# Performance work log

Measured on AMD Instinct MI355X. Metric: run time of the kernel, lower is better.

The kernel has to match this reference:

```python
import jax, jax.numpy as jnp
from jax import lax
import numpy as np

EPS = 1e-8


def setup_inputs() -> dict:
    key = jax.random.key(0)
    ks = jax.random.split(key, 9)
    B, T, E = 64, 256, 512
    L, H = 8, 512
    s = 0.05  # small init so gates are not saturated
    return {
        "x": jax.random.normal(ks[0], (B, T, E), jnp.float32),
        "w_ih": jax.random.normal(ks[1], (L, 4 * H, H), jnp.float32) * s,
        "w_hh": jax.random.normal(ks[2], (L, 4 * H, H), jnp.float32) * s,
        "b_ih": jax.random.normal(ks[3], (L, 4 * H), jnp.float32) * s,
        "b_hh": jax.random.normal(ks[4], (L, 4 * H), jnp.float32) * s,
        "ff1_w": jax.random.normal(ks[5], (H // 4, H), jnp.float32) * s,
        "ff1_b": jax.random.normal(ks[6], (H // 4,), jnp.float32) * s,
        "ff2_w": jax.random.normal(ks[7], (H // 16 * 2, H // 4), jnp.float32) * s,
        "ff2_b": jax.random.normal(ks[8], (H // 16 * 2,), jnp.float32) * s,
    }


def _lstm_layer(seq, W_ih, W_hh, bi, bh):
    # seq: [B, T, I]; PyTorch gate order: i, f, g, o
    B = seq.shape[0]
    H = W_hh.shape[1]
    pre = jnp.einsum('bti,gi->btg', seq, W_ih) + bi + bh  # [B, T, 4H]

    def step(carry, x_t):
        h, c = carry
        g = x_t + h @ W_hh.T  # [B, 4H]
        i, f, gg, o = jnp.split(g, 4, axis=-1)
        c = jax.nn.sigmoid(f) * c + jax.nn.sigmoid(i) * jnp.tanh(gg)
        h = jax.nn.sigmoid(o) * jnp.tanh(c)
        return (h, c), h

    h0 = jnp.zeros((B, H), seq.dtype)
    (hT, _), hs = lax.scan(step, (h0, h0), pre.transpose(1, 0, 2))
    return hs.transpose(1, 0, 2), hT  # [B,T,H], [B,H]


def reference(x, w_ih, w_hh, b_ih, b_hh, ff1_w, ff1_b, ff2_w, ff2_b):
    L = w_ih.shape[0]
    B = x.shape[0]
    seq = x
    finals = []
    for l in range(L):  # small fixed layer loop (sequential dependency)
        seq, hT = _lstm_layer(seq, w_ih[l], w_hh[l], b_ih[l], b_hh[l])
        finals.append(hT)
    h = jnp.stack(finals, axis=1)                # [B, L, H] == h.transpose(0,1)
    h = jax.nn.silu(h @ ff1_w.T + ff1_b)          # [B, L, H//4]
    h = h @ ff2_w.T + ff2_b                       # [B, L, H//16*2]
    h = h.reshape(B, -1)                          # [B, L*(H//16*2)]
    mean = h[:, ::2]
    log_var = h[:, 1::2]
    scale = jax.nn.softplus(log_var) + EPS        # diag of scale_tril
    return mean, scale
```

## Files before the change

kernel.cpp:

```cpp
#include <hip/hip_runtime.h>
#include <hip/hip_bf16.h>

typedef __bf16 bf16_t;
typedef __bf16 bf16x8 __attribute__((ext_vector_type(8)));
typedef float floatx4 __attribute__((ext_vector_type(4)));

#define LAYERS 8
#define BATCH  64
#define TSEQ   256
#define HDIM   512
#define GDIM   2048
#define UNITS  16
#define NROWS  64
#define WROW   1048
#define GROW   65
#define MAXM   257

#define W_OFF       0
#define W_BYTES     (NROWS * WROW * 2)
#define GATES_OFF   (W_OFF + W_BYTES)
#define GATES_BYTES (BATCH * GROW * 4)
#define C_OFF       (GATES_OFF + GATES_BYTES)
#define C_BYTES     (BATCH * UNITS * 4)
#define BIAS_OFF    (C_OFF + C_BYTES)
#define BIAS_BYTES  (NROWS * 4)
#define LDS_TOTAL   (BIAS_OFF + BIAS_BYTES)

__device__ __forceinline__ floatx4 mfma16(bf16x8 a, bf16x8 b, floatx4 c) {
    return __builtin_amdgcn_mfma_f32_16x16x32_bf16(a, b, c, 0, 0, 0);
}
__device__ __forceinline__ float sigm(float x) {
    return 1.0f / (1.0f + __expf(-x));
}
__device__ __forceinline__ unsigned pload(const unsigned* p) {
    return __hip_atomic_load(p, __ATOMIC_RELAXED, __HIP_MEMORY_SCOPE_AGENT);
}

__global__ void prep(const float* __restrict__ x, bf16_t* __restrict__ x_bf,
                     bf16_t* __restrict__ h_buf, unsigned* __restrict__ prog,
                     int M) {
    const int gtid = blockIdx.x * blockDim.x + threadIdx.x;
    const int nthr = gridDim.x * blockDim.x;
    for (int i = gtid; i < BATCH * TSEQ * HDIM; i += nthr) {
        int e = i & (HDIM - 1);
        int b = (i >> 9) & 63;
        int t = i >> 15;
        x_bf[i] = (bf16_t)x[((size_t)b * TSEQ + t) * HDIM + e];
    }
    const size_t lstride = (size_t)M * BATCH * HDIM;
    for (int i = gtid; i < LAYERS * BATCH * HDIM; i += nthr) {
        int l   = i / (BATCH * HDIM);
        int off = i % (BATCH * HDIM);
        h_buf[(size_t)l * lstride + off] = (bf16_t)0.0f;
    }
    for (int i = gtid; i < 256 * 16; i += nthr) prog[i] = 0u;
}

__global__ void lstm_main(const float* __restrict__ w_ih,
                          const float* __restrict__ w_hh,
                          const float* __restrict__ b_ih,
                          const float* __restrict__ b_hh,
                          const bf16_t* __restrict__ x_bf,
                          bf16_t* __restrict__ h_buf,
                          float*  __restrict__ finals,
                          unsigned* __restrict__ prog,
                          int M, int F)
{
    extern __shared__ char smem[];
    bf16_t* wlds  = (bf16_t*)(smem + W_OFF);
    float*  gates = (float*)(smem + GATES_OFF);
    float*  cst   = (float*)(smem + C_OFF);
    float*  bias  = (float*)(smem + BIAS_OFF);

    const int tid   = threadIdx.x;
    const int blk   = blockIdx.x;
    const int layer = blk & 7;
    const int slice = blk >> 3;
    const int u0    = slice * UNITS;
    const size_t lstride = (size_t)M * BATCH * HDIM;

    for (int r = 0; r < NROWS; ++r) {
        const int gate = ((r >> 4) * 512) + u0 + (r & 15);
        const float* srcA = w_ih + ((size_t)layer * GDIM + gate) * HDIM;
        const float* srcB = w_hh + ((size_t)layer * GDIM + gate) * HDIM;
        wlds[r * WROW + tid]       = (bf16_t)srcA[tid];
        wlds[r * WROW + 512 + tid] = (bf16_t)srcB[tid];
    }
    if (tid < NROWS) {
        const int gate = ((tid >> 4) * 512) + u0 + (tid & 15);
        bias[tid] = b_ih[layer * GDIM + gate] + b_hh[layer * GDIM + gate];
    }
    for (int i = tid; i < BATCH * UNITS; i += blockDim.x) cst[i] = 0.0f;
    __syncthreads();

    const int lane = tid & 63;
    const int wave = tid >> 6;
    const int quad = lane >> 4;
    const int l15  = lane & 15;
    const int m0   = (wave & 3) * 16;
    const int nb0  = (wave >> 2) * 32;
    const int arow = m0 + l15;
    const bf16_t* b_base0 = wlds + (size_t)(nb0 + l15) * WROW + quad * 8;
    const bf16_t* b_base1 = b_base0 + (size_t)16 * WROW;

    const int cb = tid >> 3;
    const int jp = tid & 7;
    const int i32 = tid & 31;

    for (int t = 0; t < TSEQ; ++t) {
        if (tid < 32) {
            if (layer > 0) {
                const unsigned* f = prog + ((i32 << 3) + layer - 1) * 16;
                while (pload(f) < (unsigned)(t + 1)) {}
            }
        } else if (tid >= 64 && tid < 96) {
            if (t > 0) {
                const unsigned* f = prog + ((i32 << 3) + layer) * 16;
                while (pload(f) < (unsigned)t) {}
            }
        } else if (tid >= 128 && tid < 160) {
            if (layer < 7 && t >= M - 1) {
                const unsigned* f = prog + ((i32 << 3) + layer + 1) * 16;
                while (pload(f) < (unsigned)(t - M + 2)) {}
            }
        }
        __builtin_amdgcn_fence(__ATOMIC_ACQUIRE, "workgroup");
        if ((t % F) == 0)
            __builtin_amdgcn_fence(__ATOMIC_ACQUIRE, "agent");
        __syncthreads();

        const int slot_w = (t + 1) % M;
        const int slot_o = t % M;
        const bf16_t* src_lo = (layer == 0)
            ? (x_bf + (size_t)t * BATCH * HDIM)
            : (h_buf + (size_t)(layer - 1) * lstride
                     + (size_t)slot_w * BATCH * HDIM);
        const bf16_t* src_hi =
            h_buf + (size_t)layer * lstride + (size_t)slot_o * BATCH * HDIM;

        const bf16_t* a_lo = src_lo + (size_t)arow * HDIM + quad * 8;
        const bf16_t* a_hi = src_hi + (size_t)arow * HDIM + quad * 8;

        floatx4 acc0 = {0.f, 0.f, 0.f, 0.f};
        floatx4 acc1 = {0.f, 0.f, 0.f, 0.f};

        #pragma unroll 4
        for (int kk = 0; kk < 16; ++kk) {
            bf16x8 a  = *(const bf16x8*)(a_lo + kk * 32);
            bf16x8 b0 = *(const bf16x8*)(b_base0 + kk * 32);
            bf16x8 b1 = *(const bf16x8*)(b_base1 + kk * 32);
            acc0 = mfma16(a, b0, acc0);
            acc1 = mfma16(a, b1, acc1);
        }
        #pragma unroll 4
        for (int kk = 0; kk < 16; ++kk) {
            bf16x8 a  = *(const bf16x8*)(a_hi + kk * 32);
            bf16x8 b0 = *(const bf16x8*)(b_base0 + 512 + kk * 32);
            bf16x8 b1 = *(const bf16x8*)(b_base1 + 512 + kk * 32);
            acc0 = mfma16(a, b0, acc0);
            acc1 = mfma16(a, b1, acc1);
        }

        #pragma unroll
        for (int r = 0; r < 4; ++r) {
            const int brow = m0 + quad * 4 + r;
            gates[brow * GROW + nb0 + l15]      = acc0[r];
            gates[brow * GROW + nb0 + 16 + l15] = acc1[r];
        }
        __syncthreads();

        {
            const int j0 = jp * 2, j1 = j0 + 1;
            const float* g = gates + cb * GROW;
            const float iv0 = g[j0]      + bias[j0];
            const float fv0 = g[16 + j0] + bias[16 + j0];
            const float gv0 = g[32 + j0] + bias[32 + j0];
            const float ov0 = g[48 + j0] + bias[48 + j0];
            const float iv1 = g[j1]      + bias[j1];
            const float fv1 = g[16 + j1] + bias[16 + j1];
            const float gv1 = g[32 + j1] + bias[32 + j1];
            const float ov1 = g[48 + j1] + bias[48 + j1];
            const float c0 = sigm(fv0) * cst[cb * UNITS + j0]
                           + sigm(iv0) * tanhf(gv0);
            const float c1 = sigm(fv1) * cst[cb * UNITS + j1]
                           + sigm(iv1) * tanhf(gv1);
            cst[cb * UNITS + j0] = c0;
            cst[cb * UNITS + j1] = c1;
            const float h0 = sigm(ov0) * tanhf(c0);
            const float h1 = sigm(ov1) * tanhf(c1);
            const bf16_t hb0 = (bf16_t)h0, hb1 = (bf16_t)h1;
            const uint32_t u =
                ((uint32_t)__builtin_bit_cast(unsigned short, hb1) << 16) |
                (uint32_t)__builtin_bit_cast(unsigned short, hb0);
            uint32_t* dst = (uint32_t*)(h_buf + (size_t)layer * lstride
                + ((size_t)slot_w * BATCH + cb) * HDIM + u0 + j0);
            __hip_atomic_store(dst, u, __ATOMIC_RELAXED,
                               __HIP_MEMORY_SCOPE_AGENT);
            if (t == TSEQ - 1) {
                float2 f2 = make_float2(h0, h1);
                *(float2*)(finals + ((size_t)cb * LAYERS + layer) * HDIM
                           + u0 + j0) = f2;
            }
        }
        __syncthreads();
        if (tid == 0)
            __hip_atomic_store(prog + blk * 16, (unsigned)(t + 1),
                               __ATOMIC_RELAXED, __HIP_MEMORY_SCOPE_AGENT);
    }
}

__global__ void ff_epilogue(const float* __restrict__ finals,
                            const float* __restrict__ ff1_w,
                            const float* __restrict__ ff1_b,
                            const float* __restrict__ ff2_w,
                            const float* __restrict__ ff2_b,
                            float* __restrict__ out)
{
    __shared__ float fin[HDIM];
    __shared__ float hid[128];
    const int blk = blockIdx.x;
    const int b = blk >> 3, l = blk & 7;
    const int tid = threadIdx.x;

    const float* frow = finals + ((size_t)b * LAYERS + l) * HDIM;
    for (int k = tid; k < HDIM; k += 128) fin[k] = frow[k];
    __syncthreads();

    float acc = ff1_b[tid];
    const float* w1 = ff1_w + (size_t)tid * HDIM;
    #pragma unroll 4
    for (int k = 0; k < HDIM; ++k) acc = fmaf(fin[k], w1[k], acc);
    hid[tid] = acc * (1.0f / (1.0f + __expf(-acc)));
    __syncthreads();

    if (tid < 64) {
        float o = ff2_b[tid];
        const float* w2 = ff2_w + (size_t)tid * 128;
        #pragma unroll 4
        for (int k = 0; k < 128; ++k) o = fmaf(hid[k], w2[k], o);
        const int j = l * 64 + tid;
        const int col = j >> 1;
        if ((j & 1) == 0) {
            out[b * 256 + col] = o;
        } else {
            const float sp = fmaxf(o, 0.0f) + log1pf(__expf(-fabsf(o)));
            out[64 * 256 + b * 256 + col] = sp + 1e-8f;
        }
    }
}

extern "C" void kernel_launch(void* const* d_in, const int* in_sizes, int n_in,
                              void* d_out, int out_size, void* d_ws, size_t ws_size,
                              hipStream_t stream) {
    const float* x     = (const float*)d_in[0];
    const float* w_ih  = (const float*)d_in[1];
    const float* w_hh  = (const float*)d_in[2];
    const float* b_ih  = (const float*)d_in[3];
    const float* b_hh  = (const float*)d_in[4];
    const float* ff1_w = (const float*)d_in[5];
    const float* ff1_b = (const float*)d_in[6];
    const float* ff2_w = (const float*)d_in[7];
    const float* ff2_b = (const float*)d_in[8];
    float* out = (float*)d_out;

    const size_t fixed = (size_t)TSEQ * BATCH * HDIM * 2
                       + (size_t)BATCH * LAYERS * HDIM * 4
                       + 256 * 16 * 4 + 4096;
    const size_t per_slot = (size_t)LAYERS * BATCH * HDIM * 2;
    int M = MAXM;
    if (ws_size > fixed) {
        size_t fit = (ws_size - fixed) / per_slot;
        if (fit < (size_t)M) M = (int)fit;
    }
    if (M < 5) M = 5;
    const int F = M - 1;

    char* ws = (char*)d_ws;
    bf16_t* x_bf = (bf16_t*)ws;
    size_t off = (size_t)TSEQ * BATCH * HDIM * 2;
    float* finals = (float*)(ws + off);
    off += (size_t)BATCH * LAYERS * HDIM * 4;
    unsigned* prog = (unsigned*)(ws + off);
    off += 256 * 16 * 4;
    off = (off + 255) & ~(size_t)255;
    bf16_t* h_buf = (bf16_t*)(ws + off);

    (void)in_sizes; (void)n_in; (void)out_size;

    hipFuncSetAttribute((const void*)lstm_main,
                        hipFuncAttributeMaxDynamicSharedMemorySize, LDS_TOTAL);

    prep<<<dim3(1024), dim3(256), 0, stream>>>(x, x_bf, h_buf, prog, M);

    void* args[] = {(void*)&w_ih, (void*)&w_hh, (void*)&b_ih, (void*)&b_hh,
                    (void*)&x_bf, (void*)&h_buf, (void*)&finals, (void*)&prog,
                    (void*)&M, (void*)&F};
    hipLaunchCooperativeKernel((const void*)lstm_main, dim3(256), dim3(512),
                               args, LDS_TOTAL, stream);

    ff_epilogue<<<dim3(512), dim3(128), 0, stream>>>(finals, ff1_w, ff1_b,
                                                     ff2_w, ff2_b, out);
}
```

Before: 3.036 ms.

## Split hidden-state exchange into intra-layer ring and cross-layer ring with separate flags

Separates the recurrent h exchange among blocks of the same layer (a small 16-slot ring with its own progress flags, polled using sc0 loads and stored at workgroup scope) from the cross-layer handoff (the large ring at agent scope, written only when another layer consumes it). The same-layer wait moves after the input-projection MFMA loop so the x·W_ih half overlaps with waiting on peers. The progress signal for the previous step is published early, at the start of the next step. It relies on same-layer blocks seeing each other's data through weaker scopes and cache bypass, which risks memory-ordering bugs, and it adds a second global store per element.

```diff
diff --git a/kernel.cpp b/kernel.cpp
--- a/kernel.cpp
+++ b/kernel.cpp
@@ -15,6 +15,7 @@
 #define WROW   1048
 #define GROW   65
 #define MAXM   257
+#define NSS    16
 
 #define W_OFF       0
 #define W_BYTES     (NROWS * WROW * 2)
@@ -32,13 +33,23 @@
 __device__ __forceinline__ float sigm(float x) {
     return 1.0f / (1.0f + __expf(-x));
 }
-__device__ __forceinline__ unsigned pload(const unsigned* p) {
+__device__ __forceinline__ unsigned pload_x(const unsigned* p) {
     return __hip_atomic_load(p, __ATOMIC_RELAXED, __HIP_MEMORY_SCOPE_AGENT);
 }
+__device__ __forceinline__ void pstore_x(unsigned* p, unsigned v) {
+    __hip_atomic_store(p, v, __ATOMIC_RELAXED, __HIP_MEMORY_SCOPE_AGENT);
+}
+__device__ __forceinline__ unsigned poll_s(const unsigned* p) {
+    unsigned v;
+    asm volatile("global_load_dword %0, %1, off sc0\n\t"
+                 "s_waitcnt vmcnt(0)"
+                 : "=v"(v) : "v"(p) : "memory");
+    return v;
+}
 
 __global__ void prep(const float* __restrict__ x, bf16_t* __restrict__ x_bf,
-                     bf16_t* __restrict__ h_buf, unsigned* __restrict__ prog,
-                     int M) {
+                     bf16_t* __restrict__ h_s, unsigned* __restrict__ prog_x,
+                     unsigned* __restrict__ prog_s) {
     const int gtid = blockIdx.x * blockDim.x + threadIdx.x;
     const int nthr = gridDim.x * blockDim.x;
     for (int i = gtid; i < BATCH * TSEQ * HDIM; i += nthr) {
@@ -47,13 +58,9 @@
         int t = i >> 15;
         x_bf[i] = (bf16_t)x[((size_t)b * TSEQ + t) * HDIM + e];
     }
-    const size_t lstride = (size_t)M * BATCH * HDIM;
-    for (int i = gtid; i < LAYERS * BATCH * HDIM; i += nthr) {
-        int l   = i / (BATCH * HDIM);
-        int off = i % (BATCH * HDIM);
-        h_buf[(size_t)l * lstride + off] = (bf16_t)0.0f;
-    }
-    for (int i = gtid; i < 256 * 16; i += nthr) prog[i] = 0u;
+    for (int i = gtid; i < LAYERS * NSS * BATCH * HDIM / 2; i += nthr)
+        ((unsigned*)h_s)[i] = 0u;
+    for (int i = gtid; i < 256 * 16; i += nthr) { prog_x[i] = 0u; prog_s[i] = 0u; }
 }
 
 __global__ void lstm_main(const float* __restrict__ w_ih,
@@ -61,9 +68,11 @@
                           const float* __restrict__ b_ih,
                           const float* __restrict__ b_hh,
                           const bf16_t* __restrict__ x_bf,
-                          bf16_t* __restrict__ h_buf,
+                          bf16_t* __restrict__ h_x,
+                          bf16_t* __restrict__ h_s,
                           float*  __restrict__ finals,
-                          unsigned* __restrict__ prog,
+                          unsigned* __restrict__ prog_x,
+                          unsigned* __restrict__ prog_s,
                           int M, int F)
 {
     extern __shared__ char smem[];
@@ -78,6 +87,7 @@
     const int slice = blk >> 3;
     const int u0    = slice * UNITS;
     const size_t lstride = (size_t)M * BATCH * HDIM;
+    const bool ringmode = (M < MAXM);
 
     for (int r = 0; r < NROWS; ++r) {
         const int gate = ((r >> 4) * 512) + u0 + (r & 15);
@@ -104,46 +114,33 @@
     const bf16_t* b_base1 = b_base0 + (size_t)16 * WROW;
 
     const int cb = tid >> 3;
-    const int jp = tid & 7;
+    const int jp = tid & 3 | ((tid & 7) & ~3);
     const int i32 = tid & 31;
 
     for (int t = 0; t < TSEQ; ++t) {
-        if (tid < 32) {
-            if (layer > 0) {
-                const unsigned* f = prog + ((i32 << 3) + layer - 1) * 16;
-                while (pload(f) < (unsigned)(t + 1)) {}
-            }
-        } else if (tid >= 64 && tid < 96) {
-            if (t > 0) {
-                const unsigned* f = prog + ((i32 << 3) + layer) * 16;
-                while (pload(f) < (unsigned)t) {}
-            }
-        } else if (tid >= 128 && tid < 160) {
-            if (layer < 7 && t >= M - 1) {
-                const unsigned* f = prog + ((i32 << 3) + layer + 1) * 16;
-                while (pload(f) < (unsigned)(t - M + 2)) {}
-            }
-        }
-        __builtin_amdgcn_fence(__ATOMIC_ACQUIRE, "workgroup");
-        if ((t % F) == 0)
+        if (layer > 0 && tid < 32) {
+            const unsigned* f = prog_x + ((i32 << 3) + layer - 1) * 16;
+            while ((int)(pload_x(f) - (unsigned)(t + 1)) < 0) {}
+        } else if (ringmode && layer < 7 && tid >= 128 && tid < 160 &&
+                   t >= M - 1) {
+            const unsigned* f = prog_x + ((i32 << 3) + layer + 1) * 16;
+            while ((int)(pload_x(f) - (unsigned)(t + 2 - M)) < 0) {}
+        }
+        __syncthreads();
+        if (ringmode && (t % F) == 0)
             __builtin_amdgcn_fence(__ATOMIC_ACQUIRE, "agent");
-        __syncthreads();
-
-        const int slot_w = (t + 1) % M;
-        const int slot_o = t % M;
+        if (tid == 0 && t > 0)
+            pstore_x(prog_x + blk * 16, (unsigned)t);
+
+        const int slot_lo = (t + 1) % M;
         const bf16_t* src_lo = (layer == 0)
             ? (x_bf + (size_t)t * BATCH * HDIM)
-            : (h_buf + (size_t)(layer - 1) * lstride
-                     + (size_t)slot_w * BATCH * HDIM);
-        const bf16_t* src_hi =
-            h_buf + (size_t)layer * lstride + (size_t)slot_o * BATCH * HDIM;
-
+            : (h_x + (size_t)(layer - 1) * lstride
+                   + (size_t)slot_lo * BATCH * HDIM);
         const bf16_t* a_lo = src_lo + (size_t)arow * HDIM + quad * 8;
-        const bf16_t* a_hi = src_hi + (size_t)arow * HDIM + quad * 8;
 
         floatx4 acc0 = {0.f, 0.f, 0.f, 0.f};
         floatx4 acc1 = {0.f, 0.f, 0.f, 0.f};
-
         #pragma unroll 4
         for (int kk = 0; kk < 16; ++kk) {
             bf16x8 a  = *(const bf16x8*)(a_lo + kk * 32);
@@ -152,6 +149,16 @@
             acc0 = mfma16(a, b0, acc0);
             acc1 = mfma16(a, b1, acc1);
         }
+
+        if (t > 0 && tid >= 64 && tid < 96) {
+            const unsigned* f = prog_s + ((i32 << 3) + layer) * 16;
+            while ((int)(poll_s(f) - (unsigned)t) < 0) {}
+        }
+        __syncthreads();
+
+        const bf16_t* a_hi = h_s
+            + ((size_t)layer * NSS + ((t + NSS - 1) & (NSS - 1)))
+              * BATCH * HDIM + (size_t)arow * HDIM + quad * 8;
         #pragma unroll 4
         for (int kk = 0; kk < 16; ++kk) {
             bf16x8 a  = *(const bf16x8*)(a_hi + kk * 32);
@@ -169,6 +176,7 @@
         }
         __syncthreads();
 
+        float h0, h1;
         {
             const int j0 = jp * 2, j1 = j0 + 1;
             const float* g = gates + cb * GROW;
@@ -186,27 +194,42 @@
                            + sigm(iv1) * tanhf(gv1);
             cst[cb * UNITS + j0] = c0;
             cst[cb * UNITS + j1] = c1;
-            const float h0 = sigm(ov0) * tanhf(c0);
-            const float h1 = sigm(ov1) * tanhf(c1);
+            h0 = sigm(ov0) * tanhf(c0);
+            h1 = sigm(ov1) * tanhf(c1);
             const bf16_t hb0 = (bf16_t)h0, hb1 = (bf16_t)h1;
             const uint32_t u =
                 ((uint32_t)__builtin_bit_cast(unsigned short, hb1) << 16) |
                 (uint32_t)__builtin_bit_cast(unsigned short, hb0);
-            uint32_t* dst = (uint32_t*)(h_buf + (size_t)layer * lstride
-                + ((size_t)slot_w * BATCH + cb) * HDIM + u0 + j0);
-            __hip_atomic_store(dst, u, __ATOMIC_RELAXED,
-                               __HIP_MEMORY_SCOPE_AGENT);
+            uint32_t* dst_s = (uint32_t*)(h_s
+                + ((size_t)layer * NSS + (t & (NSS - 1))) * BATCH * HDIM
+                + (size_t)cb * HDIM + u0 + j0);
+            __hip_atomic_store(dst_s, u, __ATOMIC_RELAXED,
+                               __HIP_MEMORY_SCOPE_WORKGROUP);
             if (t == TSEQ - 1) {
-                float2 f2 = make_float2(h0, h1);
                 *(float2*)(finals + ((size_t)cb * LAYERS + layer) * HDIM
-                           + u0 + j0) = f2;
+                           + u0 + j0) = make_float2(h0, h1);
             }
         }
         __syncthreads();
         if (tid == 0)
-            __hip_atomic_store(prog + blk * 16, (unsigned)(t + 1),
-                               __ATOMIC_RELAXED, __HIP_MEMORY_SCOPE_AGENT);
-    }
+            __hip_atomic_store(prog_s + blk * 16, (unsigned)(t + 1),
+                               __ATOMIC_RELAXED, __HIP_MEMORY_SCOPE_WORKGROUP);
+
+        if (layer < 7) {
+            const int j0 = jp * 2;
+            const bf16_t hb0 = (bf16_t)h0, hb1 = (bf16_t)h1;
+            const uint32_t u =
+                ((uint32_t)__builtin_bit_cast(unsigned short, hb1) << 16) |
+                (uint32_t)__builtin_bit_cast(unsigned short, hb0);
+            uint32_t* dst_x = (uint32_t*)(h_x + (size_t)layer * lstride
+                + ((size_t)((t + 1) % M) * BATCH + (size_t)cb) * HDIM
+                + u0 + j0);
+            __hip_atomic_store(dst_x, u, __ATOMIC_RELAXED,
+                               __HIP_MEMORY_SCOPE_AGENT);
+        }
+    }
+    __syncthreads();
+    if (tid == 0) pstore_x(prog_x + blk * 16, (unsigned)TSEQ);
 }
 
 __global__ void ff_epilogue(const float* __restrict__ finals,
@@ -263,38 +286,40 @@
     const float* ff2_b = (const float*)d_in[8];
     float* out = (float*)d_out;
 
-    const size_t fixed = (size_t)TSEQ * BATCH * HDIM * 2
-                       + (size_t)BATCH * LAYERS * HDIM * 4
-                       + 256 * 16 * 4 + 4096;
-    const size_t per_slot = (size_t)LAYERS * BATCH * HDIM * 2;
-    int M = MAXM;
-    if (ws_size > fixed) {
-        size_t fit = (ws_size - fixed) / per_slot;
-        if (fit < (size_t)M) M = (int)fit;
-    }
-    if (M < 5) M = 5;
-    const int F = M - 1;
-
     char* ws = (char*)d_ws;
     bf16_t* x_bf = (bf16_t*)ws;
     size_t off = (size_t)TSEQ * BATCH * HDIM * 2;
     float* finals = (float*)(ws + off);
     off += (size_t)BATCH * LAYERS * HDIM * 4;
-    unsigned* prog = (unsigned*)(ws + off);
-    off += 256 * 16 * 4;
+    unsigned* prog_x = (unsigned*)(ws + off);  off += 256 * 16 * 4;
+    unsigned* prog_s = (unsigned*)(ws + off);  off += 256 * 16 * 4;
     off = (off + 255) & ~(size_t)255;
-    bf16_t* h_buf = (bf16_t*)(ws + off);
+    bf16_t* h_s = (bf16_t*)(ws + off);
+    off += (size_t)LAYERS * NSS * BATCH * HDIM * 2;
+    off = (off + 255) & ~(size_t)255;
+
+    const size_t per_slot = (size_t)LAYERS * BATCH * HDIM * 2;
+    int M = MAXM;
+    if (ws_size > off) {
+        size_t fit = (ws_size - off) / per_slot;
+        if (fit < (size_t)M) M = (int)fit;
+    } else {
+        M = 5;
+    }
+    if (M < 5) M = 5;
+    const int F = M - 1;
+    bf16_t* h_x = (bf16_t*)(ws + off);
 
     (void)in_sizes; (void)n_in; (void)out_size;
 
     hipFuncSetAttribute((const void*)lstm_main,
                         hipFuncAttributeMaxDynamicSharedMemorySize, LDS_TOTAL);
 
-    prep<<<dim3(1024), dim3(256), 0, stream>>>(x, x_bf, h_buf, prog, M);
+    prep<<<dim3(1024), dim3(256), 0, stream>>>(x, x_bf, h_s, prog_x, prog_s);
 
     void* args[] = {(void*)&w_ih, (void*)&w_hh, (void*)&b_ih, (void*)&b_hh,
-                    (void*)&x_bf, (void*)&h_buf, (void*)&finals, (void*)&prog,
-                    (void*)&M, (void*)&F};
+                    (void*)&x_bf, (void*)&h_x, (void*)&h_s, (void*)&finals,
+                    (void*)&prog_x, (void*)&prog_s, (void*)&M, (void*)&F};
     hipLaunchCooperativeKernel((const void*)lstm_main, dim3(256), dim3(512),
                                args, LDS_TOTAL, stream);
 
```

Result: faster. 2.678 ms (-11.8%).
